# Optimization experiments

Hardware: AMD Instinct MI355X
Metric: run time of the kernel (lower is better)

Reference implementation:

```python
import jax, jax.numpy as jnp
import numpy as np

BN_EPS = 1e-5
KS = 4  # 4x4 morphology kernel (np.ones((4,4)))


def _bn(x, gamma, beta, mean, var):
    # eval-mode BatchNorm2d over channel dim 1 of [B,C,H,W]
    inv = jax.lax.rsqrt(var + BN_EPS)
    return (x - mean[None, :, None, None]) * (gamma * inv)[None, :, None, None] + beta[None, :, None, None]


def _erosion_to_dilate(m):
    # m: [B,1,H,W]; threshold > 0.3, then 4x4 binary erosion (min-pool) and
    # dilation (max-pool), SAME padding; border padded so it does not erode/dilate,
    # matching cv2's default morphology border behavior.
    z = jnp.where(m > 0.3, 1.0, 0.0).astype(m.dtype)
    er = jax.lax.reduce_window(z, jnp.array(1.0, z.dtype), jax.lax.min,
                               (1, 1, KS, KS), (1, 1, 1, 1), 'SAME')
    di = jax.lax.reduce_window(z, jnp.array(0.0, z.dtype), jax.lax.max,
                               (1, 1, KS, KS), (1, 1, 1, 1), 'SAME')
    # [maske, background, maskd] along channel dim -> [B,3,H,W]
    return jnp.concatenate([er, 1.0 - di, di - er], axis=1)


def setup_inputs() -> dict:
    key = jax.random.key(0)
    ks = jax.random.split(key, 8)
    B, C, H, W = 8, 256, 128, 128
    feature = jax.random.normal(ks[0], (B, C, H, W), dtype=jnp.float32)
    m = jax.random.uniform(ks[1], (B, 1, H, W), dtype=jnp.float32)
    w_feat = jax.random.normal(ks[2], (C, C), dtype=jnp.float32) * 0.02
    w_out = jax.random.normal(ks[3], (C, 2 * C), dtype=jnp.float32) * 0.02
    bn_f_gamma = jnp.ones((C,), jnp.float32)
    bn_f_beta = jnp.zeros((C,), jnp.float32)
    bn_f_mean = jnp.zeros((C,), jnp.float32)
    bn_f_var = jnp.ones((C,), jnp.float32)
    bn_o_gamma = jnp.ones((C,), jnp.float32)
    bn_o_beta = jnp.zeros((C,), jnp.float32)
    bn_o_mean = jnp.zeros((C,), jnp.float32)
    bn_o_var = jnp.ones((C,), jnp.float32)
    return {"feature": feature, "m": m, "w_feat": w_feat,
            "bn_f_gamma": bn_f_gamma, "bn_f_beta": bn_f_beta,
            "bn_f_mean": bn_f_mean, "bn_f_var": bn_f_var,
            "w_out": w_out, "bn_o_gamma": bn_o_gamma, "bn_o_beta": bn_o_beta,
            "bn_o_mean": bn_o_mean, "bn_o_var": bn_o_var}


def reference(feature, m, w_feat, bn_f_gamma, bn_f_beta, bn_f_mean, bn_f_var,
              w_out, bn_o_gamma, bn_o_beta, bn_o_mean, bn_o_var):
    B, C, H, W = feature.shape
    HW = H * W
    m = jax.nn.relu(m)
    # erosion_to_dilate is computed via numpy/OpenCV in the original -> detached
    fbu = jax.lax.stop_gradient(_erosion_to_dilate(m)).reshape(B, 3, HW)
    f1 = feature.reshape(B, C, HW)
    # mid_feature = fbu @ feature^T : [B,3,C]
    mid = jnp.einsum('bkn,bcn->bkc', fbu, f1)
    # conv1x1_feature: 1x1 conv (no bias) + eval BN, NO relu (BasicConv2d.forward)
    cf = _bn(jnp.einsum('bchw,oc->bohw', feature, w_feat),
             bn_f_gamma, bn_f_beta, bn_f_mean, bn_f_var).reshape(B, C, HW)
    mid1 = jnp.einsum('bkc,bcn->bkn', mid, cf)          # [B,3,HW]
    mid2 = jnp.einsum('bkc,bkn->bcn', mid, mid1)        # [B,C,HW]
    mid2 = mid2.reshape(B, C, H, W)
    cat = jnp.concatenate([feature, mid2], axis=1)      # [B,2C,H,W]
    out = _bn(jnp.einsum('bchw,oc->bohw', cat, w_out),
              bn_o_gamma, bn_o_beta, bn_o_mean, bn_o_var)
    return out
```

## Files before the change

kernel.cpp:

```cpp
#include <hip/hip_runtime.h>

#define HW 16384

typedef unsigned short ushort_t;
typedef unsigned int uint32;
typedef __attribute__((ext_vector_type(8))) short short8;
typedef __attribute__((ext_vector_type(4))) float floatx4;

__device__ __forceinline__ ushort_t f2bf(float x) {
  uint32 u = __float_as_uint(x);
  u += 0x7fffu + ((u >> 16) & 1u);
  return (ushort_t)(u >> 16);
}

__global__ __launch_bounds__(256) void k_masks(const float* __restrict__ m,
                                               float* __restrict__ er,
                                               float* __restrict__ di) {
  int idx = blockIdx.x * 256 + threadIdx.x;
  int b = idx >> 14;
  int p = idx & (HW - 1);
  int i = p >> 7, j = p & 127;
  const float* mb = m + (b << 14);
  float ermn = 1.f, dimx = 0.f;
  for (int di_ = -1; di_ <= 2; ++di_) {
    int ii = i + di_;
    if (ii < 0 || ii >= 128) continue;
    for (int dj = -1; dj <= 2; ++dj) {
      int jj = j + dj;
      if (jj < 0 || jj >= 128) continue;
      float z = ((double)mb[ii * 128 + jj] > 0.3) ? 1.f : 0.f;
      ermn = fminf(ermn, z);
      dimx = fmaxf(dimx, z);
    }
  }
  er[idx] = ermn;
  di[idx] = dimx;
}

__global__ __launch_bounds__(256) void k_midsums(const float* __restrict__ f,
                                                 const float* __restrict__ er,
                                                 const float* __restrict__ di,
                                                 float* __restrict__ out) {
  int b = blockIdx.x >> 8;
  int c = blockIdx.x & 255;
  const float4* f4 = (const float4*)(f + ((size_t)(b * 256 + c) << 14));
  const float4* e4 = (const float4*)(er + ((size_t)b << 14));
  const float4* d4 = (const float4*)(di + ((size_t)b << 14));
  int t = threadIdx.x;
  float se = 0.f, st = 0.f, sd = 0.f;
#pragma unroll
  for (int it = 0; it < 16; ++it) {
    int i = it * 256 + t;
    float4 x = f4[i];
    float4 e = e4[i];
    float4 dd = d4[i];
    st += (x.x + x.y) + (x.z + x.w);
    se += x.x * e.x + x.y * e.y + x.z * e.z + x.w * e.w;
    sd += x.x * dd.x + x.y * dd.y + x.z * dd.z + x.w * dd.w;
  }
  __shared__ float red[3][4];
  for (int off = 32; off; off >>= 1) {
    se += __shfl_down(se, off);
    st += __shfl_down(st, off);
    sd += __shfl_down(sd, off);
  }
  int wave = t >> 6;
  if ((t & 63) == 0) { red[0][wave] = se; red[1][wave] = st; red[2][wave] = sd; }
  __syncthreads();
  if (t == 0) {
    se = red[0][0] + red[0][1] + red[0][2] + red[0][3];
    st = red[1][0] + red[1][1] + red[1][2] + red[1][3];
    sd = red[2][0] + red[2][1] + red[2][2] + red[2][3];
    float* o = out + (size_t)(b * 256 + c) * 3;
    o[0] = se; o[1] = st; o[2] = sd;
  }
}

__global__ __launch_bounds__(256) void k_prep(
    const float* __restrict__ midsums, const float* __restrict__ wfeat,
    const float* __restrict__ gf, const float* __restrict__ bfp,
    const float* __restrict__ mfp, const float* __restrict__ vfp,
    const float* __restrict__ wout, const float* __restrict__ g2,
    const float* __restrict__ b2p, const float* __restrict__ m2p,
    const float* __restrict__ v2p, ushort_t* __restrict__ Wbf,
    float* __restrict__ bias_eff) {
  const int b = blockIdx.x;
  const int t = threadIdx.x;
  __shared__ float mid[3][256];
  __shared__ float msc[3][256];
  __shared__ float tl[256], s2l[256], t2l[256];
  __shared__ float ul[3];
  __shared__ float Bm[3][256];
  __shared__ float bias2[256];
  __shared__ float A2[256][3];

  {
    const float* ms = midsums + (size_t)(b * 256 + t) * 3;
    float se = ms[0], st = ms[1], sd = ms[2];
    float m0 = se, m1 = st - sd, m2v = sd - se;
    mid[0][t] = m0; mid[1][t] = m1; mid[2][t] = m2v;
    float s = gf[t] * rsqrtf(vfp[t] + 1e-5f);
    tl[t] = bfp[t] - mfp[t] * s;
    msc[0][t] = m0 * s; msc[1][t] = m1 * s; msc[2][t] = m2v * s;
    float s2 = g2[t] * rsqrtf(v2p[t] + 1e-5f);
    s2l[t] = s2;
    t2l[t] = b2p[t] - m2p[t] * s2;
  }
  __syncthreads();
  if (t < 3) {
    float u = 0.f;
    for (int c = 0; c < 256; ++c) u += mid[t][c] * tl[c];
    ul[t] = u;
  }
  {
    float b0 = 0.f, b1 = 0.f, b2v = 0.f;
    for (int o = 0; o < 256; ++o) {
      float wfv = wfeat[o * 256 + t];
      b0 += msc[0][o] * wfv;
      b1 += msc[1][o] * wfv;
      b2v += msc[2][o] * wfv;
    }
    Bm[0][t] = b0; Bm[1][t] = b1; Bm[2][t] = b2v;
  }
  __syncthreads();
  bias2[t] = mid[0][t] * ul[0] + mid[1][t] * ul[1] + mid[2][t] * ul[2];
  __syncthreads();
  {
    const float4* w2 = (const float4*)(wout + t * 512 + 256);
    float a0 = 0.f, a1 = 0.f, a2v = 0.f, bb = 0.f;
    for (int cq = 0; cq < 64; ++cq) {
      float4 wv = w2[cq];
      int c = cq * 4;
      a0 += wv.x * mid[0][c] + wv.y * mid[0][c + 1] + wv.z * mid[0][c + 2] + wv.w * mid[0][c + 3];
      a1 += wv.x * mid[1][c] + wv.y * mid[1][c + 1] + wv.z * mid[1][c + 2] + wv.w * mid[1][c + 3];
      a2v += wv.x * mid[2][c] + wv.y * mid[2][c + 1] + wv.z * mid[2][c + 2] + wv.w * mid[2][c + 3];
      bb += wv.x * bias2[c] + wv.y * bias2[c + 1] + wv.z * bias2[c + 2] + wv.w * bias2[c + 3];
    }
    A2[t][0] = a0; A2[t][1] = a1; A2[t][2] = a2v;
    bias_eff[b * 256 + t] = s2l[t] * bb + t2l[t];
  }
  __syncthreads();
  {
    float bm0 = Bm[0][t], bm1 = Bm[1][t], bm2 = Bm[2][t];
    ushort_t* Wb = Wbf + ((size_t)b << 16);
    for (int o = 0; o < 256; ++o) {
      float wv = wout[o * 512 + t];
      float val = s2l[o] * (wv + A2[o][0] * bm0 + A2[o][1] * bm1 + A2[o][2] * bm2);
      Wb[o * 256 + t] = f2bf(val);
    }
  }
}

__global__ __launch_bounds__(256) void k_gemm(const float* __restrict__ f,
                                              const ushort_t* __restrict__ Wbf,
                                              const float* __restrict__ bias,
                                              float* __restrict__ out) {
  const int b = blockIdx.x >> 8;
  const int n0 = (blockIdx.x & 255) * 64;
  const int wv = threadIdx.x >> 6;
  const int lane = threadIdx.x & 63;
  const int l15 = lane & 15;
  const int quad = lane >> 4;
  const int obase = wv * 64;
  const float* fb = f + ((size_t)b << 22);
  const ushort_t* Wb = Wbf + ((size_t)b << 16);
  const float* biasb = bias + (b << 8);

  floatx4 acc[4][4];
#pragma unroll
  for (int ot = 0; ot < 4; ++ot) {
#pragma unroll
    for (int r = 0; r < 4; ++r) {
      float bv = biasb[obase + ot * 16 + quad * 4 + r];
#pragma unroll
      for (int nt = 0; nt < 4; ++nt) acc[ot][nt][r] = bv;
    }
  }

  for (int kc = 0; kc < 256; kc += 32) {
    short8 a[4];
#pragma unroll
    for (int ot = 0; ot < 4; ++ot)
      a[ot] = *(const short8*)(Wb + (size_t)(obase + ot * 16 + l15) * 256 + kc + quad * 8);
    short8 bfr[4];
#pragma unroll
    for (int j = 0; j < 8; ++j) {
      const float* p = fb + (size_t)(kc + quad * 8 + j) * HW + n0 + l15;
#pragma unroll
      for (int nt = 0; nt < 4; ++nt) bfr[nt][j] = (short)f2bf(p[nt * 16]);
    }
#pragma unroll
    for (int ot = 0; ot < 4; ++ot)
#pragma unroll
      for (int nt = 0; nt < 4; ++nt)
        acc[ot][nt] = __builtin_amdgcn_mfma_f32_16x16x32_bf16(a[ot], bfr[nt], acc[ot][nt], 0, 0, 0);
  }

  float* ob = out + ((size_t)b << 22);
#pragma unroll
  for (int ot = 0; ot < 4; ++ot)
#pragma unroll
    for (int nt = 0; nt < 4; ++nt)
#pragma unroll
      for (int r = 0; r < 4; ++r)
        ob[(size_t)(obase + ot * 16 + quad * 4 + r) * HW + n0 + nt * 16 + l15] = acc[ot][nt][r];
}

extern "C" void kernel_launch(void* const* d_in, const int* in_sizes, int n_in,
                              void* d_out, int out_size, void* d_ws, size_t ws_size,
                              hipStream_t stream) {
  (void)in_sizes; (void)n_in; (void)out_size; (void)ws_size;
  const float* feature = (const float*)d_in[0];
  const float* m = (const float*)d_in[1];
  const float* w_feat = (const float*)d_in[2];
  const float* gf = (const float*)d_in[3];
  const float* bf = (const float*)d_in[4];
  const float* mf = (const float*)d_in[5];
  const float* vf = (const float*)d_in[6];
  const float* w_out = (const float*)d_in[7];
  const float* g2 = (const float*)d_in[8];
  const float* b2 = (const float*)d_in[9];
  const float* m2 = (const float*)d_in[10];
  const float* v2 = (const float*)d_in[11];
  float* out = (float*)d_out;

  float* ws = (float*)d_ws;
  float* er = ws;
  float* di = ws + 131072;
  float* midsums = ws + 262144;
  float* bias_eff = ws + 268288;
  ushort_t* Wbf = (ushort_t*)((char*)d_ws + 1081344);

  hipLaunchKernelGGL(k_masks, dim3(512), dim3(256), 0, stream, m, er, di);
  hipLaunchKernelGGL(k_midsums, dim3(2048), dim3(256), 0, stream, feature, er, di, midsums);
  hipLaunchKernelGGL(k_prep, dim3(8), dim3(256), 0, stream, midsums, w_feat,
                     gf, bf, mf, vf, w_out, g2, b2, m2, v2, Wbf, bias_eff);
  hipLaunchKernelGGL(k_gemm, dim3(2048), dim3(256), 0, stream, feature, Wbf, bias_eff, out);
}
```

Before: 356.3 us.

## Fuse bf16 channel-packing into the mask-sum pass and feed packed operands to GEMM

The mask-weighted channel-sum kernel now also converts the fp32 feature map to bf16, packed 8 channels per pixel. It writes this into a workspace buffer and reduces its partial sums with atomics into a buffer zeroed by the mask kernel. The GEMM then loads its B operand as one 16-byte vector per tile instead of eight strided fp32 loads plus conversions. The feature tensor is still read twice, but the GEMM's second read drops from fp32 to half-size bf16 with coalesced access. The cost is an extra 64MB write of packed data and atomic contention on the midsums. Unroll pragmas are also added in the small prep kernel.

```diff
diff --git a/kernel.cpp b/kernel.cpp
--- a/kernel.cpp
+++ b/kernel.cpp
@@ -15,8 +15,10 @@
 
 __global__ __launch_bounds__(256) void k_masks(const float* __restrict__ m,
                                                float* __restrict__ er,
-                                               float* __restrict__ di) {
+                                               float* __restrict__ di,
+                                               float* __restrict__ midsums) {
   int idx = blockIdx.x * 256 + threadIdx.x;
+  if (blockIdx.x < 24) midsums[idx] = 0.f;
   int b = idx >> 14;
   int p = idx & (HW - 1);
   int i = p >> 7, j = p & 127;
@@ -37,42 +39,70 @@
   di[idx] = dimx;
 }
 
-__global__ __launch_bounds__(256) void k_midsums(const float* __restrict__ f,
-                                                 const float* __restrict__ er,
-                                                 const float* __restrict__ di,
-                                                 float* __restrict__ out) {
-  int b = blockIdx.x >> 8;
-  int c = blockIdx.x & 255;
-  const float4* f4 = (const float4*)(f + ((size_t)(b * 256 + c) << 14));
-  const float4* e4 = (const float4*)(er + ((size_t)b << 14));
-  const float4* d4 = (const float4*)(di + ((size_t)b << 14));
-  int t = threadIdx.x;
-  float se = 0.f, st = 0.f, sd = 0.f;
-#pragma unroll
-  for (int it = 0; it < 16; ++it) {
-    int i = it * 256 + t;
-    float4 x = f4[i];
-    float4 e = e4[i];
-    float4 dd = d4[i];
-    st += (x.x + x.y) + (x.z + x.w);
-    se += x.x * e.x + x.y * e.y + x.z * e.z + x.w * e.w;
-    sd += x.x * dd.x + x.y * dd.y + x.z * dd.z + x.w * dd.w;
-  }
-  __shared__ float red[3][4];
-  for (int off = 32; off; off >>= 1) {
-    se += __shfl_down(se, off);
-    st += __shfl_down(st, off);
-    sd += __shfl_down(sd, off);
-  }
-  int wave = t >> 6;
-  if ((t & 63) == 0) { red[0][wave] = se; red[1][wave] = st; red[2][wave] = sd; }
-  __syncthreads();
-  if (t == 0) {
-    se = red[0][0] + red[0][1] + red[0][2] + red[0][3];
-    st = red[1][0] + red[1][1] + red[1][2] + red[1][3];
-    sd = red[2][0] + red[2][1] + red[2][2] + red[2][3];
-    float* o = out + (size_t)(b * 256 + c) * 3;
-    o[0] = se; o[1] = st; o[2] = sd;
+__global__ __launch_bounds__(256) void k_pack(const float* __restrict__ f,
+                                              const float* __restrict__ er,
+                                              const float* __restrict__ di,
+                                              ushort_t* __restrict__ packed,
+                                              float* __restrict__ midsums) {
+  const int bx = blockIdx.x;
+  const int b = bx >> 8;
+  const int c8 = (bx >> 3) & 31;
+  const int nc = bx & 7;
+  const int t = threadIdx.x;
+  const float* fb = f + ((size_t)b << 22) + ((size_t)(c8 * 8) << 14);
+  const float* erb = er + ((size_t)b << 14);
+  const float* dib = di + ((size_t)b << 14);
+  ushort_t* pk = packed + (((size_t)(b * 32 + c8)) << 14) * 8;
+
+  float se[8], st[8], sd[8];
+#pragma unroll
+  for (int i = 0; i < 8; ++i) { se[i] = 0.f; st[i] = 0.f; sd[i] = 0.f; }
+
+#pragma unroll
+  for (int j = 0; j < 2; ++j) {
+    int n = nc * 2048 + j * 1024 + t * 4;
+    float4 e = *(const float4*)(erb + n);
+    float4 dd = *(const float4*)(dib + n);
+    float4 row[8];
+#pragma unroll
+    for (int i = 0; i < 8; ++i) row[i] = *(const float4*)(fb + ((size_t)i << 14) + n);
+#pragma unroll
+    for (int i = 0; i < 8; ++i) {
+      st[i] += (row[i].x + row[i].y) + (row[i].z + row[i].w);
+      se[i] += row[i].x * e.x + row[i].y * e.y + row[i].z * e.z + row[i].w * e.w;
+      sd[i] += row[i].x * dd.x + row[i].y * dd.y + row[i].z * dd.z + row[i].w * dd.w;
+    }
+#pragma unroll
+    for (int r = 0; r < 4; ++r) {
+      uint32 w0 = (uint32)f2bf(((const float*)&row[0])[r]) |
+                  ((uint32)f2bf(((const float*)&row[1])[r]) << 16);
+      uint32 w1 = (uint32)f2bf(((const float*)&row[2])[r]) |
+                  ((uint32)f2bf(((const float*)&row[3])[r]) << 16);
+      uint32 w2 = (uint32)f2bf(((const float*)&row[4])[r]) |
+                  ((uint32)f2bf(((const float*)&row[5])[r]) << 16);
+      uint32 w3 = (uint32)f2bf(((const float*)&row[6])[r]) |
+                  ((uint32)f2bf(((const float*)&row[7])[r]) << 16);
+      uint4 pkd; pkd.x = w0; pkd.y = w1; pkd.z = w2; pkd.w = w3;
+      *(uint4*)(pk + (size_t)(n + r) * 8) = pkd;
+    }
+  }
+
+#pragma unroll
+  for (int i = 0; i < 8; ++i) {
+    for (int off = 32; off; off >>= 1) {
+      se[i] += __shfl_down(se[i], off);
+      st[i] += __shfl_down(st[i], off);
+      sd[i] += __shfl_down(sd[i], off);
+    }
+  }
+  if ((t & 63) == 0) {
+    float* msb = midsums + (size_t)(b * 256 + c8 * 8) * 3;
+#pragma unroll
+    for (int i = 0; i < 8; ++i) {
+      atomicAdd(&msb[i * 3 + 0], se[i]);
+      atomicAdd(&msb[i * 3 + 1], st[i]);
+      atomicAdd(&msb[i * 3 + 2], sd[i]);
+    }
   }
 }
 
@@ -109,11 +139,13 @@
   __syncthreads();
   if (t < 3) {
     float u = 0.f;
+#pragma unroll 8
     for (int c = 0; c < 256; ++c) u += mid[t][c] * tl[c];
     ul[t] = u;
   }
   {
     float b0 = 0.f, b1 = 0.f, b2v = 0.f;
+#pragma unroll 8
     for (int o = 0; o < 256; ++o) {
       float wfv = wfeat[o * 256 + t];
       b0 += msc[0][o] * wfv;
@@ -128,6 +160,7 @@
   {
     const float4* w2 = (const float4*)(wout + t * 512 + 256);
     float a0 = 0.f, a1 = 0.f, a2v = 0.f, bb = 0.f;
+#pragma unroll 4
     for (int cq = 0; cq < 64; ++cq) {
       float4 wv = w2[cq];
       int c = cq * 4;
@@ -143,6 +176,7 @@
   {
     float bm0 = Bm[0][t], bm1 = Bm[1][t], bm2 = Bm[2][t];
     ushort_t* Wb = Wbf + ((size_t)b << 16);
+#pragma unroll 8
     for (int o = 0; o < 256; ++o) {
       float wv = wout[o * 512 + t];
       float val = s2l[o] * (wv + A2[o][0] * bm0 + A2[o][1] * bm1 + A2[o][2] * bm2);
@@ -151,7 +185,7 @@
   }
 }
 
-__global__ __launch_bounds__(256) void k_gemm(const float* __restrict__ f,
+__global__ __launch_bounds__(256) void k_gemm(const ushort_t* __restrict__ packed,
                                               const ushort_t* __restrict__ Wbf,
                                               const float* __restrict__ bias,
                                               float* __restrict__ out) {
@@ -162,7 +196,7 @@
   const int l15 = lane & 15;
   const int quad = lane >> 4;
   const int obase = wv * 64;
-  const float* fb = f + ((size_t)b << 22);
+  const ushort_t* pkb = packed + (((size_t)(b * 32)) << 14) * 8;
   const ushort_t* Wb = Wbf + ((size_t)b << 16);
   const float* biasb = bias + (b << 8);
 
@@ -184,11 +218,9 @@
       a[ot] = *(const short8*)(Wb + (size_t)(obase + ot * 16 + l15) * 256 + kc + quad * 8);
     short8 bfr[4];
 #pragma unroll
-    for (int j = 0; j < 8; ++j) {
-      const float* p = fb + (size_t)(kc + quad * 8 + j) * HW + n0 + l15;
-#pragma unroll
-      for (int nt = 0; nt < 4; ++nt) bfr[nt][j] = (short)f2bf(p[nt * 16]);
-    }
+    for (int nt = 0; nt < 4; ++nt)
+      bfr[nt] = *(const short8*)(pkb + (((size_t)((kc >> 3) + quad)) << 14) * 8 +
+                                 (size_t)(n0 + nt * 16 + l15) * 8);
 #pragma unroll
     for (int ot = 0; ot < 4; ++ot)
 #pragma unroll
@@ -224,16 +256,17 @@
   const float* v2 = (const float*)d_in[11];
   float* out = (float*)d_out;
 
-  float* ws = (float*)d_ws;
-  float* er = ws;
-  float* di = ws + 131072;
-  float* midsums = ws + 262144;
-  float* bias_eff = ws + 268288;
-  ushort_t* Wbf = (ushort_t*)((char*)d_ws + 1081344);
-
-  hipLaunchKernelGGL(k_masks, dim3(512), dim3(256), 0, stream, m, er, di);
-  hipLaunchKernelGGL(k_midsums, dim3(2048), dim3(256), 0, stream, feature, er, di, midsums);
+  char* wsb = (char*)d_ws;
+  float* er = (float*)wsb;
+  float* di = (float*)(wsb + (512 << 10));
+  float* midsums = (float*)(wsb + (1 << 20));
+  float* bias_eff = (float*)(wsb + (1 << 20) + (32 << 10));
+  ushort_t* Wbf = (ushort_t*)(wsb + (2 << 20));
+  ushort_t* packed = (ushort_t*)(wsb + (4 << 20));
+
+  hipLaunchKernelGGL(k_masks, dim3(512), dim3(256), 0, stream, m, er, di, midsums);
+  hipLaunchKernelGGL(k_pack, dim3(2048), dim3(256), 0, stream, feature, er, di, packed, midsums);
   hipLaunchKernelGGL(k_prep, dim3(8), dim3(256), 0, stream, midsums, w_feat,
                      gf, bf, mf, vf, w_out, g2, b2, m2, v2, Wbf, bias_eff);
-  hipLaunchKernelGGL(k_gemm, dim3(2048), dim3(256), 0, stream, feature, Wbf, bias_eff, out);
-}
+  hipLaunchKernelGGL(k_gemm, dim3(2048), dim3(256), 0, stream, packed, Wbf, bias_eff, out);
+}
```

Measured after the change: 370.0 us. 3.9% more time.

## Stage feature tiles through LDS with coalesced float4 loads in GEMM

Applied to the files above, without the earlier changes.

The GEMM kernel now loads 64-channel by 64-column feature tiles with coalesced float4 global loads into a padded LDS buffer, then builds the bf16 B fragments from LDS. Before, each lane issued scattered scalar global loads. The change aims to cut global load instruction count and improve coalescing, at the cost of extra LDS traffic and two barriers per k-chunk. It also adds unroll pragmas to the prep kernel loops and realigns the workspace offsets to power-of-two boundaries.

```diff
diff --git a/kernel.cpp b/kernel.cpp
--- a/kernel.cpp
+++ b/kernel.cpp
@@ -1,6 +1,7 @@
 #include <hip/hip_runtime.h>
 
 #define HW 16384
+#define LDSP 66
 
 typedef unsigned short ushort_t;
 typedef unsigned int uint32;
@@ -109,11 +110,13 @@
   __syncthreads();
   if (t < 3) {
     float u = 0.f;
+#pragma unroll 8
     for (int c = 0; c < 256; ++c) u += mid[t][c] * tl[c];
     ul[t] = u;
   }
   {
     float b0 = 0.f, b1 = 0.f, b2v = 0.f;
+#pragma unroll 8
     for (int o = 0; o < 256; ++o) {
       float wfv = wfeat[o * 256 + t];
       b0 += msc[0][o] * wfv;
@@ -128,6 +131,7 @@
   {
     const float4* w2 = (const float4*)(wout + t * 512 + 256);
     float a0 = 0.f, a1 = 0.f, a2v = 0.f, bb = 0.f;
+#pragma unroll 4
     for (int cq = 0; cq < 64; ++cq) {
       float4 wv = w2[cq];
       int c = cq * 4;
@@ -143,6 +147,7 @@
   {
     float bm0 = Bm[0][t], bm1 = Bm[1][t], bm2 = Bm[2][t];
     ushort_t* Wb = Wbf + ((size_t)b << 16);
+#pragma unroll 8
     for (int o = 0; o < 256; ++o) {
       float wv = wout[o * 512 + t];
       float val = s2l[o] * (wv + A2[o][0] * bm0 + A2[o][1] * bm1 + A2[o][2] * bm2);
@@ -155,10 +160,12 @@
                                               const ushort_t* __restrict__ Wbf,
                                               const float* __restrict__ bias,
                                               float* __restrict__ out) {
+  __shared__ float lds[64 * LDSP];
   const int b = blockIdx.x >> 8;
   const int n0 = (blockIdx.x & 255) * 64;
-  const int wv = threadIdx.x >> 6;
-  const int lane = threadIdx.x & 63;
+  const int t = threadIdx.x;
+  const int wv = t >> 6;
+  const int lane = t & 63;
   const int l15 = lane & 15;
   const int quad = lane >> 4;
   const int obase = wv * 64;
@@ -166,6 +173,9 @@
   const ushort_t* Wb = Wbf + ((size_t)b << 16);
   const float* biasb = bias + (b << 8);
 
+  const int c_loc = t >> 2;
+  const int f4c = t & 3;
+
   floatx4 acc[4][4];
 #pragma unroll
   for (int ot = 0; ot < 4; ++ot) {
@@ -177,23 +187,40 @@
     }
   }
 
-  for (int kc = 0; kc < 256; kc += 32) {
-    short8 a[4];
-#pragma unroll
-    for (int ot = 0; ot < 4; ++ot)
-      a[ot] = *(const short8*)(Wb + (size_t)(obase + ot * 16 + l15) * 256 + kc + quad * 8);
-    short8 bfr[4];
-#pragma unroll
-    for (int j = 0; j < 8; ++j) {
-      const float* p = fb + (size_t)(kc + quad * 8 + j) * HW + n0 + l15;
-#pragma unroll
-      for (int nt = 0; nt < 4; ++nt) bfr[nt][j] = (short)f2bf(p[nt * 16]);
-    }
-#pragma unroll
-    for (int ot = 0; ot < 4; ++ot)
-#pragma unroll
-      for (int nt = 0; nt < 4; ++nt)
-        acc[ot][nt] = __builtin_amdgcn_mfma_f32_16x16x32_bf16(a[ot], bfr[nt], acc[ot][nt], 0, 0, 0);
+  for (int kc = 0; kc < 256; kc += 64) {
+    const float4* gsrc = (const float4*)(fb + (size_t)(kc + c_loc) * HW + n0);
+    float4 v[4];
+#pragma unroll
+    for (int k = 0; k < 4; ++k) v[k] = gsrc[f4c + 4 * k];
+    if (kc) __syncthreads();
+    float* dst = &lds[c_loc * LDSP];
+#pragma unroll
+    for (int k = 0; k < 4; ++k) {
+      int col = (f4c + 4 * k) * 4;
+      *(float2*)(dst + col) = make_float2(v[k].x, v[k].y);
+      *(float2*)(dst + col + 2) = make_float2(v[k].z, v[k].w);
+    }
+    __syncthreads();
+#pragma unroll
+    for (int ks = 0; ks < 2; ++ks) {
+      short8 a[4];
+#pragma unroll
+      for (int ot = 0; ot < 4; ++ot)
+        a[ot] = *(const short8*)(Wb + (size_t)(obase + ot * 16 + l15) * 256 +
+                                 kc + ks * 32 + quad * 8);
+      short8 bfr[4];
+#pragma unroll
+      for (int nt = 0; nt < 4; ++nt) {
+#pragma unroll
+        for (int j = 0; j < 8; ++j)
+          bfr[nt][j] = (short)f2bf(lds[(ks * 32 + quad * 8 + j) * LDSP + nt * 16 + l15]);
+      }
+#pragma unroll
+      for (int ot = 0; ot < 4; ++ot)
+#pragma unroll
+        for (int nt = 0; nt < 4; ++nt)
+          acc[ot][nt] = __builtin_amdgcn_mfma_f32_16x16x32_bf16(a[ot], bfr[nt], acc[ot][nt], 0, 0, 0);
+    }
   }
 
   float* ob = out + ((size_t)b << 22);
@@ -224,12 +251,12 @@
   const float* v2 = (const float*)d_in[11];
   float* out = (float*)d_out;
 
-  float* ws = (float*)d_ws;
-  float* er = ws;
-  float* di = ws + 131072;
-  float* midsums = ws + 262144;
-  float* bias_eff = ws + 268288;
-  ushort_t* Wbf = (ushort_t*)((char*)d_ws + 1081344);
+  char* wsb = (char*)d_ws;
+  float* er = (float*)wsb;
+  float* di = (float*)(wsb + (512 << 10));
+  float* midsums = (float*)(wsb + (1 << 20));
+  float* bias_eff = (float*)(wsb + (1 << 20) + (32 << 10));
+  ushort_t* Wbf = (ushort_t*)(wsb + (2 << 20));
 
   hipLaunchKernelGGL(k_masks, dim3(512), dim3(256), 0, stream, m, er, di);
   hipLaunchKernelGGL(k_midsums, dim3(2048), dim3(256), 0, stream, feature, er, di, midsums);
```

Result: faster. 346.7 us (-2.7%).
